# Performance work log

Measured on AMD Instinct MI355X. Metric: run time of the kernel, lower is better.

Reference implementation:

```python
import jax, jax.numpy as jnp
import numpy as np


def setup_inputs() -> dict:
    key = jax.random.key(0)
    k1, k2 = jax.random.split(key)
    B = 64
    K = 4096
    latent_shape = (8, 250, 16)
    latent = jax.random.normal(k1, (B,) + latent_shape, dtype=jnp.float32)
    codebook = jax.random.normal(k2, (K,) + latent_shape, dtype=jnp.float32)
    usage_count = jnp.zeros((K,), dtype=jnp.float32)
    return {"latent": latent, "codebook": codebook, "usage_count": usage_count}


def reference(latent, codebook, usage_count):
    B = latent.shape[0]
    K = codebook.shape[0]
    latent_flat = latent.reshape(B, -1).astype(jnp.float32)      # [B, D]
    codebook_flat = codebook.reshape(K, -1).astype(jnp.float32)  # [K, D]

    x2 = jnp.sum(latent_flat * latent_flat, axis=1, keepdims=True)      # [B, 1]
    c2 = jnp.sum(codebook_flat * codebook_flat, axis=1)[None, :]        # [1, K]
    xc = jnp.einsum('bd,kd->bk', latent_flat, codebook_flat)            # [B, K]
    distances = jnp.sqrt(jnp.maximum(x2 + c2 - 2.0 * xc, 0.0))          # [B, K]

    indices = jnp.argmin(distances, axis=1)                             # [B] int
    min_distances = jnp.take_along_axis(distances, indices[:, None], axis=1)[:, 0]

    quantized = codebook[indices].astype(latent.dtype)                  # [B, *latent_shape]

    # scatter-add usage count update (handles duplicate indices)
    new_usage_count = usage_count.at[indices].add(1.0)

    return quantized, indices, min_distances, new_usage_count
```

## Files before the change

### kernel.cpp

```cpp
#include <hip/hip_runtime.h>
#include <math.h>

#define D      32000
#define BNUM   64
#define KNUM   4096
#define TN     64
#define BK     64
#define LDK    72

typedef __attribute__((ext_vector_type(8)))  short  short8;
typedef __attribute__((ext_vector_type(16))) float  floatx16;

__device__ __forceinline__ unsigned short f32_bf16_rne(float f) {
    unsigned u = __float_as_uint(f);
    u += 0x7fff + ((u >> 16) & 1);
    return (unsigned short)(u >> 16);
}
__device__ __forceinline__ float bf16_f32(unsigned short h) {
    return __uint_as_float(((unsigned)h) << 16);
}

__global__ __launch_bounds__(256) void dist_mfma(
    const float* __restrict__ latent, const float* __restrict__ codebook,
    float* __restrict__ ws_xc, float* __restrict__ ws_c2, int dper)
{
    __shared__ __align__(16) unsigned short xs_hi[BNUM * LDK];
    __shared__ __align__(16) unsigned short xs_lo[BNUM * LDK];
    __shared__ __align__(16) unsigned short cs_hi[TN * LDK];
    __shared__ __align__(16) unsigned short cs_lo[TN * LDK];

    const int tid  = threadIdx.x;
    const int k0   = blockIdx.x * TN;
    const int d0b  = blockIdx.y * dper;
    const int nst  = dper / BK;

    const int col4  = tid & 15;
    const int rbase = tid >> 4;
    const float* aptr = latent   + (size_t)rbase * D + d0b + col4 * 4;
    const float* bptr = codebook + (size_t)(k0 + rbase) * D + d0b + col4 * 4;

    const int wave = tid >> 6, lane = tid & 63;
    const int lr = lane & 31, lh = lane >> 5;
    const int mh = (wave & 1) * 32;
    const int nh = (wave >> 1) * 32;
    const int aoff = (mh + lr) * LDK + lh * 8;
    const int boff = (nh + lr) * LDK + lh * 8;

    floatx16 acc;
#pragma unroll
    for (int i = 0; i < 16; i++) acc[i] = 0.f;
    float c2p[4] = {0.f, 0.f, 0.f, 0.f};

    float4 pa[4], pb[4];
#pragma unroll
    for (int p = 0; p < 4; p++) {
        pa[p] = *(const float4*)(aptr + (size_t)(16 * p) * D);
        pb[p] = *(const float4*)(bptr + (size_t)(16 * p) * D);
    }

    for (int s = 0; s < nst; ++s) {
#pragma unroll
        for (int p = 0; p < 4; p++)
            c2p[p] += pb[p].x * pb[p].x + pb[p].y * pb[p].y +
                      pb[p].z * pb[p].z + pb[p].w * pb[p].w;

        __syncthreads();
#pragma unroll
        for (int p = 0; p < 4; p++) {
            const int wo = (rbase + 16 * p) * LDK + col4 * 4;
            ushort4 h, l;
            h.x = f32_bf16_rne(pa[p].x); l.x = f32_bf16_rne(pa[p].x - bf16_f32(h.x));
            h.y = f32_bf16_rne(pa[p].y); l.y = f32_bf16_rne(pa[p].y - bf16_f32(h.y));
            h.z = f32_bf16_rne(pa[p].z); l.z = f32_bf16_rne(pa[p].z - bf16_f32(h.z));
            h.w = f32_bf16_rne(pa[p].w); l.w = f32_bf16_rne(pa[p].w - bf16_f32(h.w));
            *(ushort4*)(xs_hi + wo) = h;
            *(ushort4*)(xs_lo + wo) = l;
            h.x = f32_bf16_rne(pb[p].x); l.x = f32_bf16_rne(pb[p].x - bf16_f32(h.x));
            h.y = f32_bf16_rne(pb[p].y); l.y = f32_bf16_rne(pb[p].y - bf16_f32(h.y));
            h.z = f32_bf16_rne(pb[p].z); l.z = f32_bf16_rne(pb[p].z - bf16_f32(h.z));
            h.w = f32_bf16_rne(pb[p].w); l.w = f32_bf16_rne(pb[p].w - bf16_f32(h.w));
            *(ushort4*)(cs_hi + wo) = h;
            *(ushort4*)(cs_lo + wo) = l;
        }
        __syncthreads();

        if (s + 1 < nst) {
            const int doff = (s + 1) * BK;
#pragma unroll
            for (int p = 0; p < 4; p++) {
                pa[p] = *(const float4*)(aptr + (size_t)(16 * p) * D + doff);
                pb[p] = *(const float4*)(bptr + (size_t)(16 * p) * D + doff);
            }
        }

#pragma unroll
        for (int ks = 0; ks < 4; ++ks) {
            const short8 ah = *(const short8*)(xs_hi + aoff + ks * 16);
            const short8 al = *(const short8*)(xs_lo + aoff + ks * 16);
            const short8 bh = *(const short8*)(cs_hi + boff + ks * 16);
            const short8 bl = *(const short8*)(cs_lo + boff + ks * 16);
            acc = __builtin_amdgcn_mfma_f32_32x32x16_bf16(ah, bh, acc, 0, 0, 0);
            acc = __builtin_amdgcn_mfma_f32_32x32x16_bf16(ah, bl, acc, 0, 0, 0);
            acc = __builtin_amdgcn_mfma_f32_32x32x16_bf16(al, bh, acc, 0, 0, 0);
        }
    }

    const int split = blockIdx.y;
#pragma unroll
    for (int r = 0; r < 16; ++r) {
        const int row = (r & 3) + 8 * (r >> 2) + 4 * lh;
        const int b = mh + row;
        ws_xc[((size_t)split * BNUM + b) * KNUM + (k0 + nh + lr)] = acc[r];
    }

#pragma unroll
    for (int p = 0; p < 4; ++p) {
        float v = c2p[p];
        v += __shfl_xor(v, 1);
        v += __shfl_xor(v, 2);
        v += __shfl_xor(v, 4);
        v += __shfl_xor(v, 8);
        if ((lane & 15) == 0)
            atomicAdd(ws_c2 + k0 + rbase + 16 * p, v);
    }
}

__global__ __launch_bounds__(256) void argmin_k(
    const float* __restrict__ latent, const float* __restrict__ ws_xc,
    const float* __restrict__ ws_c2, const float* __restrict__ usage_in,
    float* __restrict__ out_idx, float* __restrict__ out_mind,
    float* __restrict__ out_usage, int* __restrict__ ws_idx, int dsplit)
{
    const int b = blockIdx.x, tid = threadIdx.x;
    __shared__ float svals[256];
    __shared__ int   sidx[256];

    float s = 0.f;
    const float4* lf4 = (const float4*)(latent + (size_t)b * D);
    for (int i = tid; i < D / 4; i += 256) {
        const float4 v = lf4[i];
        s += v.x * v.x + v.y * v.y + v.z * v.z + v.w * v.w;
    }
    svals[tid] = s;
    __syncthreads();
    for (int off = 128; off > 0; off >>= 1) {
        if (tid < off) svals[tid] += svals[tid + off];
        __syncthreads();
    }
    const float x2 = svals[0];
    __syncthreads();

    float best = 3.402823466e38f;
    int   bi   = 0;
    for (int k = tid; k < KNUM; k += 256) {
        float xc = 0.f;
        for (int sdx = 0; sdx < dsplit; sdx++)
            xc += ws_xc[((size_t)sdx * BNUM + b) * KNUM + k];
        const float sc = ws_c2[k] - 2.f * xc;
        if (sc < best) { best = sc; bi = k; }
    }
    svals[tid] = best; sidx[tid] = bi;
    __syncthreads();
    for (int off = 128; off > 0; off >>= 1) {
        if (tid < off) {
            const float ov = svals[tid + off];
            const int   oi = sidx[tid + off];
            if (ov < svals[tid] || (ov == svals[tid] && oi < sidx[tid])) {
                svals[tid] = ov; sidx[tid] = oi;
            }
        }
        __syncthreads();
    }
    if (tid == 0) {
        const int k = sidx[0];
        out_mind[b] = sqrtf(fmaxf(x2 + svals[0], 0.f));
        out_idx[b]  = (float)k;
        ws_idx[b]   = k;
    }
    if (tid < 64) out_usage[b * 64 + tid] = usage_in[b * 64 + tid];
}

__global__ __launch_bounds__(256) void gather_k(
    const float* __restrict__ codebook, const int* __restrict__ ws_idx,
    float* __restrict__ out_q, float* __restrict__ out_usage)
{
    const int b = blockIdx.x, part = blockIdx.y, tid = threadIdx.x;
    const int k = ws_idx[b];
    const int n4 = D / 4 / 4;
    const float4* src = (const float4*)(codebook + (size_t)k * D) + part * n4;
    float4*       dst = (float4*)(out_q + (size_t)b * D) + part * n4;
    for (int i = tid; i < n4; i += 256) dst[i] = src[i];
    if (part == 0 && tid == 0) atomicAdd(out_usage + k, 1.0f);
}

extern "C" void kernel_launch(void* const* d_in, const int* in_sizes, int n_in,
                              void* d_out, int out_size, void* d_ws, size_t ws_size,
                              hipStream_t stream)
{
    const float* latent   = (const float*)d_in[0];
    const float* codebook = (const float*)d_in[1];
    const float* usage    = (const float*)d_in[2];

    float* out_q     = (float*)d_out;
    float* out_idx   = out_q + (size_t)BNUM * D;
    float* out_mind  = out_idx + BNUM;
    float* out_usage = out_mind + BNUM;

    int dsplit = 10;
    if (ws_size < (size_t)dsplit * BNUM * KNUM * 4 + KNUM * 4 + 256) dsplit = 4;
    const int dper = D / dsplit;

    float* ws_xc  = (float*)d_ws;
    float* ws_c2  = ws_xc + (size_t)dsplit * BNUM * KNUM;
    int*   ws_idx = (int*)(ws_c2 + KNUM);

    hipMemsetAsync(ws_c2, 0, KNUM * sizeof(float), stream);
    dist_mfma<<<dim3(KNUM / TN, dsplit), 256, 0, stream>>>(latent, codebook, ws_xc, ws_c2, dper);
    argmin_k<<<BNUM, 256, 0, stream>>>(latent, ws_xc, ws_c2, usage,
                                       out_idx, out_mind, out_usage, ws_idx, dsplit);
    gather_k<<<dim3(BNUM, 4), 256, 0, stream>>>(codebook, ws_idx, out_q, out_usage);
}
```

Measured before the change: 766.0 us.

## Double-buffer codebook prefetch, relax barriers, raise split-K, and split argmin

The distance GEMM loop now keeps two register buffers for codebook tiles and prefetches two stages ahead. It replaces __syncthreads with raw s_barrier plus a waitcnt that only drains LDS traffic, so outstanding global loads stay in flight across the barrier. It also sets a min-blocks-per-CU launch bound and doubles the D split from 10 to 20 for more blocks. The argmin is split into a 4-way partial kernel plus a finalize kernel to spread the reduction over more blocks. The costs are more register pressure, a larger split-K workspace to sum, and an extra kernel launch.

```diff
diff --git a/kernel.cpp b/kernel.cpp
--- a/kernel.cpp
+++ b/kernel.cpp
@@ -19,8 +19,22 @@
 __device__ __forceinline__ float bf16_f32(unsigned short h) {
     return __uint_as_float(((unsigned)h) << 16);
 }
-
-__global__ __launch_bounds__(256) void dist_mfma(
+__device__ __forceinline__ void cvt_hl(const float4 v, ushort4* h, ushort4* l) {
+    h->x = f32_bf16_rne(v.x); l->x = f32_bf16_rne(v.x - bf16_f32(h->x));
+    h->y = f32_bf16_rne(v.y); l->y = f32_bf16_rne(v.y - bf16_f32(h->y));
+    h->z = f32_bf16_rne(v.z); l->z = f32_bf16_rne(v.z - bf16_f32(h->z));
+    h->w = f32_bf16_rne(v.w); l->w = f32_bf16_rne(v.w - bf16_f32(h->w));
+}
+
+__device__ __forceinline__ void barrier_arrive() {
+    __builtin_amdgcn_s_barrier();
+}
+__device__ __forceinline__ void barrier_lds() {
+    __builtin_amdgcn_s_waitcnt(0xc07f);
+    __builtin_amdgcn_s_barrier();
+}
+
+__global__ __launch_bounds__(256, 4) void dist_mfma(
     const float* __restrict__ latent, const float* __restrict__ codebook,
     float* __restrict__ ws_xc, float* __restrict__ ws_c2, int dper)
 {
@@ -51,59 +65,70 @@
     for (int i = 0; i < 16; i++) acc[i] = 0.f;
     float c2p[4] = {0.f, 0.f, 0.f, 0.f};
 
-    float4 pa[4], pb[4];
-#pragma unroll
-    for (int p = 0; p < 4; p++) {
-        pa[p] = *(const float4*)(aptr + (size_t)(16 * p) * D);
-        pb[p] = *(const float4*)(bptr + (size_t)(16 * p) * D);
-    }
-
-    for (int s = 0; s < nst; ++s) {
-#pragma unroll
-        for (int p = 0; p < 4; p++)
-            c2p[p] += pb[p].x * pb[p].x + pb[p].y * pb[p].y +
-                      pb[p].z * pb[p].z + pb[p].w * pb[p].w;
-
-        __syncthreads();
-#pragma unroll
-        for (int p = 0; p < 4; p++) {
-            const int wo = (rbase + 16 * p) * LDK + col4 * 4;
-            ushort4 h, l;
-            h.x = f32_bf16_rne(pa[p].x); l.x = f32_bf16_rne(pa[p].x - bf16_f32(h.x));
-            h.y = f32_bf16_rne(pa[p].y); l.y = f32_bf16_rne(pa[p].y - bf16_f32(h.y));
-            h.z = f32_bf16_rne(pa[p].z); l.z = f32_bf16_rne(pa[p].z - bf16_f32(h.z));
-            h.w = f32_bf16_rne(pa[p].w); l.w = f32_bf16_rne(pa[p].w - bf16_f32(h.w));
-            *(ushort4*)(xs_hi + wo) = h;
-            *(ushort4*)(xs_lo + wo) = l;
-            h.x = f32_bf16_rne(pb[p].x); l.x = f32_bf16_rne(pb[p].x - bf16_f32(h.x));
-            h.y = f32_bf16_rne(pb[p].y); l.y = f32_bf16_rne(pb[p].y - bf16_f32(h.y));
-            h.z = f32_bf16_rne(pb[p].z); l.z = f32_bf16_rne(pb[p].z - bf16_f32(h.z));
-            h.w = f32_bf16_rne(pb[p].w); l.w = f32_bf16_rne(pb[p].w - bf16_f32(h.w));
-            *(ushort4*)(cs_hi + wo) = h;
-            *(ushort4*)(cs_lo + wo) = l;
-        }
-        __syncthreads();
-
-        if (s + 1 < nst) {
-            const int doff = (s + 1) * BK;
-#pragma unroll
-            for (int p = 0; p < 4; p++) {
-                pa[p] = *(const float4*)(aptr + (size_t)(16 * p) * D + doff);
-                pb[p] = *(const float4*)(bptr + (size_t)(16 * p) * D + doff);
-            }
-        }
-
-#pragma unroll
-        for (int ks = 0; ks < 4; ++ks) {
-            const short8 ah = *(const short8*)(xs_hi + aoff + ks * 16);
-            const short8 al = *(const short8*)(xs_lo + aoff + ks * 16);
-            const short8 bh = *(const short8*)(cs_hi + boff + ks * 16);
-            const short8 bl = *(const short8*)(cs_lo + boff + ks * 16);
-            acc = __builtin_amdgcn_mfma_f32_32x32x16_bf16(ah, bh, acc, 0, 0, 0);
-            acc = __builtin_amdgcn_mfma_f32_32x32x16_bf16(ah, bl, acc, 0, 0, 0);
-            acc = __builtin_amdgcn_mfma_f32_32x32x16_bf16(al, bh, acc, 0, 0, 0);
-        }
-    }
+    float4 pa[4], pbA[4], pbB[4];
+
+#define LOADA(DST, S)                                                          \
+    if ((S) < nst) {                                                           \
+        const size_t _o = (size_t)(S) * BK;                                    \
+        _Pragma("unroll")                                                      \
+        for (int p = 0; p < 4; p++)                                            \
+            DST[p] = *(const float4*)(aptr + (size_t)(16 * p) * D + _o);       \
+    }
+#define LOADB(DST, S)                                                          \
+    if ((S) < nst) {                                                           \
+        const size_t _o = (size_t)(S) * BK;                                    \
+        _Pragma("unroll")                                                      \
+        for (int p = 0; p < 4; p++)                                            \
+            DST[p] = *(const float4*)(bptr + (size_t)(16 * p) * D + _o);       \
+    }
+
+#define STAGE(PBC, S)                                                          \
+    {                                                                          \
+        _Pragma("unroll")                                                      \
+        for (int p = 0; p < 4; p++)                                            \
+            c2p[p] += PBC[p].x * PBC[p].x + PBC[p].y * PBC[p].y +              \
+                      PBC[p].z * PBC[p].z + PBC[p].w * PBC[p].w;               \
+        barrier_arrive();                     \
+        _Pragma("unroll")                                                      \
+        for (int p = 0; p < 4; p++) {                                          \
+            const int wo = (rbase + 16 * p) * LDK + col4 * 4;                  \
+            ushort4 h, l;                                                      \
+            cvt_hl(pa[p], &h, &l);                                             \
+            *(ushort4*)(xs_hi + wo) = h;                                       \
+            *(ushort4*)(xs_lo + wo) = l;                                       \
+            cvt_hl(PBC[p], &h, &l);                                            \
+            *(ushort4*)(cs_hi + wo) = h;                                       \
+            *(ushort4*)(cs_lo + wo) = l;                                       \
+        }                                                                      \
+        LOADA(pa, (S) + 1);       \
+        LOADB(PBC, (S) + 2);        \
+        barrier_lds();                                                         \
+        _Pragma("unroll")                                                      \
+        for (int ks = 0; ks < 4; ++ks) {                                       \
+            const short8 ah = *(const short8*)(xs_hi + aoff + ks * 16);        \
+            const short8 al = *(const short8*)(xs_lo + aoff + ks * 16);        \
+            const short8 bh = *(const short8*)(cs_hi + boff + ks * 16);        \
+            const short8 bl = *(const short8*)(cs_lo + boff + ks * 16);        \
+            acc = __builtin_amdgcn_mfma_f32_32x32x16_bf16(ah, bh, acc, 0,0,0); \
+            acc = __builtin_amdgcn_mfma_f32_32x32x16_bf16(ah, bl, acc, 0,0,0); \
+            acc = __builtin_amdgcn_mfma_f32_32x32x16_bf16(al, bh, acc, 0,0,0); \
+        }                                                                      \
+    }
+
+    LOADA(pa, 0);
+    LOADB(pbA, 0);
+    LOADB(pbB, 1);
+
+    int s = 0;
+    for (; s + 1 < nst; s += 2) {
+        STAGE(pbA, s);
+        STAGE(pbB, s + 1);
+    }
+    if (s < nst) STAGE(pbA, s);
+
+#undef STAGE
+#undef LOADA
+#undef LOADB
 
     const int split = blockIdx.y;
 #pragma unroll
@@ -125,15 +150,46 @@
     }
 }
 
-__global__ __launch_bounds__(256) void argmin_k(
-    const float* __restrict__ latent, const float* __restrict__ ws_xc,
-    const float* __restrict__ ws_c2, const float* __restrict__ usage_in,
+__global__ __launch_bounds__(256) void argmin_part(
+    const float* __restrict__ ws_xc, const float* __restrict__ ws_c2,
+    float* __restrict__ ws_bscore, int* __restrict__ ws_bidx, int dsplit)
+{
+    const int b = blockIdx.x, kc = blockIdx.y, tid = threadIdx.x;
+    __shared__ float sv[256];
+    __shared__ int   si[256];
+
+    float best = 3.402823466e38f;
+    int   bi   = 0;
+    for (int k = kc * 1024 + tid; k < (kc + 1) * 1024; k += 256) {
+        float xc = 0.f;
+        for (int s = 0; s < dsplit; s++)
+            xc += ws_xc[((size_t)s * BNUM + b) * KNUM + k];
+        const float sc = ws_c2[k] - 2.f * xc;
+        if (sc < best) { best = sc; bi = k; }
+    }
+    sv[tid] = best; si[tid] = bi;
+    __syncthreads();
+    for (int off = 128; off > 0; off >>= 1) {
+        if (tid < off) {
+            const float ov = sv[tid + off];
+            const int   oi = si[tid + off];
+            if (ov < sv[tid] || (ov == sv[tid] && oi < si[tid])) {
+                sv[tid] = ov; si[tid] = oi;
+            }
+        }
+        __syncthreads();
+    }
+    if (tid == 0) { ws_bscore[b * 4 + kc] = sv[0]; ws_bidx[b * 4 + kc] = si[0]; }
+}
+
+__global__ __launch_bounds__(256) void finalize_k(
+    const float* __restrict__ latent, const float* __restrict__ ws_bscore,
+    const int* __restrict__ ws_bidx, const float* __restrict__ usage_in,
     float* __restrict__ out_idx, float* __restrict__ out_mind,
-    float* __restrict__ out_usage, int* __restrict__ ws_idx, int dsplit)
+    float* __restrict__ out_usage, int* __restrict__ ws_idx)
 {
     const int b = blockIdx.x, tid = threadIdx.x;
-    __shared__ float svals[256];
-    __shared__ int   sidx[256];
+    __shared__ float sv[256];
 
     float s = 0.f;
     const float4* lf4 = (const float4*)(latent + (size_t)b * D);
@@ -141,41 +197,23 @@
         const float4 v = lf4[i];
         s += v.x * v.x + v.y * v.y + v.z * v.z + v.w * v.w;
     }
-    svals[tid] = s;
+    sv[tid] = s;
     __syncthreads();
     for (int off = 128; off > 0; off >>= 1) {
-        if (tid < off) svals[tid] += svals[tid + off];
+        if (tid < off) sv[tid] += sv[tid + off];
         __syncthreads();
     }
-    const float x2 = svals[0];
-    __syncthreads();
-
-    float best = 3.402823466e38f;
-    int   bi   = 0;
-    for (int k = tid; k < KNUM; k += 256) {
-        float xc = 0.f;
-        for (int sdx = 0; sdx < dsplit; sdx++)
-            xc += ws_xc[((size_t)sdx * BNUM + b) * KNUM + k];
-        const float sc = ws_c2[k] - 2.f * xc;
-        if (sc < best) { best = sc; bi = k; }
-    }
-    svals[tid] = best; sidx[tid] = bi;
-    __syncthreads();
-    for (int off = 128; off > 0; off >>= 1) {
-        if (tid < off) {
-            const float ov = svals[tid + off];
-            const int   oi = sidx[tid + off];
-            if (ov < svals[tid] || (ov == svals[tid] && oi < sidx[tid])) {
-                svals[tid] = ov; sidx[tid] = oi;
-            }
+    if (tid == 0) {
+        const float x2 = sv[0];
+        float best = ws_bscore[b * 4];
+        int   bi   = ws_bidx[b * 4];
+        for (int kc = 1; kc < 4; kc++) {
+            const float v = ws_bscore[b * 4 + kc];
+            if (v < best) { best = v; bi = ws_bidx[b * 4 + kc]; }
         }
-        __syncthreads();
-    }
-    if (tid == 0) {
-        const int k = sidx[0];
-        out_mind[b] = sqrtf(fmaxf(x2 + svals[0], 0.f));
-        out_idx[b]  = (float)k;
-        ws_idx[b]   = k;
+        out_mind[b] = sqrtf(fmaxf(x2 + best, 0.f));
+        out_idx[b]  = (float)bi;
+        ws_idx[b]   = bi;
     }
     if (tid < 64) out_usage[b * 64 + tid] = usage_in[b * 64 + tid];
 }
@@ -206,17 +244,21 @@
     float* out_mind  = out_idx + BNUM;
     float* out_usage = out_mind + BNUM;
 
-    int dsplit = 10;
-    if (ws_size < (size_t)dsplit * BNUM * KNUM * 4 + KNUM * 4 + 256) dsplit = 4;
+    int dsplit = 20;
+    if (ws_size < ((size_t)dsplit * BNUM * KNUM + KNUM + 4 * BNUM * 2 + BNUM) * 4 + 256)
+        dsplit = 4;
     const int dper = D / dsplit;
 
-    float* ws_xc  = (float*)d_ws;
-    float* ws_c2  = ws_xc + (size_t)dsplit * BNUM * KNUM;
-    int*   ws_idx = (int*)(ws_c2 + KNUM);
+    float* ws_xc     = (float*)d_ws;
+    float* ws_c2     = ws_xc + (size_t)dsplit * BNUM * KNUM;
+    float* ws_bscore = ws_c2 + KNUM;
+    int*   ws_bidx   = (int*)(ws_bscore + 4 * BNUM);
+    int*   ws_idx    = ws_bidx + 4 * BNUM;
 
     hipMemsetAsync(ws_c2, 0, KNUM * sizeof(float), stream);
     dist_mfma<<<dim3(KNUM / TN, dsplit), 256, 0, stream>>>(latent, codebook, ws_xc, ws_c2, dper);
-    argmin_k<<<BNUM, 256, 0, stream>>>(latent, ws_xc, ws_c2, usage,
-                                       out_idx, out_mind, out_usage, ws_idx, dsplit);
+    argmin_part<<<dim3(BNUM, 4), 256, 0, stream>>>(ws_xc, ws_c2, ws_bscore, ws_bidx, dsplit);
+    finalize_k<<<BNUM, 256, 0, stream>>>(latent, ws_bscore, ws_bidx, usage,
+                                         out_idx, out_mind, out_usage, ws_idx);
     gather_k<<<dim3(BNUM, 4), 256, 0, stream>>>(codebook, ws_idx, out_q, out_usage);
 }
```

New measurement: 756.3 us. No clear change (-1.3%).
